# Optimization experiments

Measured on AMD Instinct MI355X. Metric: run time of the kernel, lower is better.

## Reference

```python
import jax, jax.numpy as jnp
import numpy as np

K_H, K_W = 3, 3
STRIDE, PAD = 1, 1
GN_GROUPS = 32
EPS = 1e-5


def setup_inputs() -> dict:
    key = jax.random.key(0)
    k1, k2, k3 = jax.random.split(key, 3)
    B, C, H, W = 4, 256, 64, 64
    Cout = 256
    x = jax.random.normal(k1, (B, C, H, W), jnp.float32)
    offset = jax.random.normal(k2, (B, 2 * K_H * K_W, H, W), jnp.float32)
    weight = jax.random.normal(k3, (Cout, C, K_H, K_W), jnp.float32) * 0.02
    gamma = jnp.ones((Cout,), jnp.float32)
    beta = jnp.zeros((Cout,), jnp.float32)
    return {"x": x, "offset": offset, "weight": weight, "gamma": gamma, "beta": beta}


def _deform_conv(x, offset, weight):
    B, C, H, W = x.shape
    Cout = weight.shape[0]
    K = K_H * K_W
    Ho = (H + 2 * PAD - K_H) // STRIDE + 1
    Wo = (W + 2 * PAD - K_W) // STRIDE + 1
    ky, kx = jnp.meshgrid(jnp.arange(K_H), jnp.arange(K_W), indexing='ij')
    ky = ky.reshape(K).astype(x.dtype)
    kx = kx.reshape(K).astype(x.dtype)
    # base sampling positions per kernel tap
    py_base = (jnp.arange(Ho) * STRIDE - PAD).astype(x.dtype)[None, :] + ky[:, None]  # [K,Ho]
    px_base = (jnp.arange(Wo) * STRIDE - PAD).astype(x.dtype)[None, :] + kx[:, None]  # [K,Wo]
    off = offset.reshape(B, K, 2, Ho, Wo)  # mmcv layout: (dy, dx) pairs per tap
    py = py_base[None, :, :, None] + off[:, :, 0]  # [B,K,Ho,Wo]
    px = px_base[None, :, None, :] + off[:, :, 1]  # [B,K,Ho,Wo]
    y0 = jnp.floor(py)
    x0 = jnp.floor(px)
    ly = py - y0
    lx = px - x0
    xf = x.reshape(B, C, H * W)

    def gather(yi, xi):
        valid = (yi >= 0) & (yi <= H - 1) & (xi >= 0) & (xi <= W - 1)
        yc = jnp.clip(yi, 0, H - 1).astype(jnp.int32)
        xc = jnp.clip(xi, 0, W - 1).astype(jnp.int32)
        idx = yc * W + xc  # [B,K,Ho,Wo]
        vals = jax.vmap(lambda xb, ib: xb[:, ib])(xf, idx)  # [B,C,K,Ho,Wo]
        return vals * valid[:, None].astype(x.dtype)

    g00 = gather(y0, x0)
    g01 = gather(y0, x0 + 1)
    g10 = gather(y0 + 1, x0)
    g11 = gather(y0 + 1, x0 + 1)
    wy = ly[:, None]  # [B,1,K,Ho,Wo]
    wx = lx[:, None]
    val = ((1 - wy) * (1 - wx) * g00 + (1 - wy) * wx * g01
           + wy * (1 - wx) * g10 + wy * wx * g11)  # [B,C,K,Ho,Wo]
    return jnp.einsum('bckhw,ock->bohw', val, weight.reshape(Cout, C, K))


def reference(x, offset, weight, gamma, beta):
    y = _deform_conv(x, offset, weight)  # [B,Cout,Ho,Wo]
    B, C, H, W = y.shape
    yg = y.reshape(B, GN_GROUPS, C // GN_GROUPS, H, W)
    mean = jnp.mean(yg, axis=(2, 3, 4), keepdims=True)
    var = jnp.var(yg, axis=(2, 3, 4), keepdims=True)
    yn = ((yg - mean) * jax.lax.rsqrt(var + EPS)).reshape(B, C, H, W)
    out = yn * gamma[None, :, None, None] + beta[None, :, None, None]
    return jax.nn.relu(out)
```

## Files before the change

### kernel.cpp

```cpp
#include <hip/hip_runtime.h>

typedef unsigned short ushort_t;
typedef __bf16 bf16x8 __attribute__((ext_vector_type(8)));
typedef float f32x4 __attribute__((ext_vector_type(4)));
typedef void __attribute__((address_space(1))) gvoid_t;
typedef void __attribute__((address_space(3))) lvoid_t;

__device__ __forceinline__ float bflo(unsigned u) { return __builtin_bit_cast(float, u << 16); }
__device__ __forceinline__ float bfhi(unsigned u) { return __builtin_bit_cast(float, u & 0xffff0000u); }
__device__ __forceinline__ float bf2f(ushort_t v) {
  return __builtin_bit_cast(float, ((unsigned)v) << 16);
}
__device__ __forceinline__ unsigned f2bf_bits(float f) {
  unsigned u = __builtin_bit_cast(unsigned, f);
  return (u + 0x7fffu + ((u >> 16) & 1u)) >> 16;
}
__device__ __forceinline__ ushort_t f2bf(float f) { return (ushort_t)f2bf_bits(f); }

__global__ __launch_bounds__(256) void k_prep(const float* __restrict__ x,
                                              const float* __restrict__ w,
                                              ushort_t* __restrict__ xt,
                                              ushort_t* __restrict__ wb,
                                              float* __restrict__ stats) {
  const int gid = blockIdx.x;
  const int t = threadIdx.x;
  if (gid >= 1024) {
    if (gid == 1024) stats[t] = 0.f;
    const int idx = (gid - 1024) * 256 + t;
    const float* src = w + (size_t)idx * 9;
    #pragma unroll
    for (int k = 0; k < 9; ++k)
      wb[(k << 16) + idx] = f2bf(src[k]);
    return;
  }
  __shared__ ushort_t tile[64][68];
  const int b = gid >> 8;
  const int ct = (gid >> 6) & 3;
  const int pt = gid & 63;
  const float* xb = x + ((size_t)(b * 256 + ct * 64)) * 4096 + pt * 64;
  #pragma unroll
  for (int i = 0; i < 16; ++i) {
    const int idx = t + 256 * i;
    const int c_l = idx >> 6, p_l = idx & 63;
    tile[c_l][p_l] = f2bf(xb[(size_t)c_l * 4096 + p_l]);
  }
  __syncthreads();
  ushort_t* xo = xt + ((size_t)(b * 4096 + pt * 64)) * 256 + ct * 64;
  #pragma unroll
  for (int i = 0; i < 16; ++i) {
    const int idx = t + 256 * i;
    const int p_l = idx >> 6, c_l = idx & 63;
    xo[(size_t)p_l * 256 + c_l] = tile[c_l][p_l];
  }
}

struct SMeta {
  float w00, w01, w10, w11;
  int i00, i01, i10, i11;
};
__device__ __forceinline__ SMeta meta_for(int h, int gw, int k, float oy, float ox) {
  SMeta m;
  const float py = (float)(h - 1 + k / 3) + oy;
  const float px = (float)(gw - 1 + k % 3) + ox;
  const float fy = floorf(py), fx = floorf(px);
  const float ly = py - fy, lx = px - fx;
  const int iy0 = (int)fy, ix0 = (int)fx;
  const float vy0 = (iy0 >= 0 && iy0 < 64) ? 1.f : 0.f;
  const float vy1 = (iy0 >= -1 && iy0 < 63) ? 1.f : 0.f;
  const float vx0 = (ix0 >= 0 && ix0 < 64) ? 1.f : 0.f;
  const float vx1 = (ix0 >= -1 && ix0 < 63) ? 1.f : 0.f;
  m.w00 = (1.f - ly) * (1.f - lx) * vy0 * vx0;
  m.w01 = (1.f - ly) * lx * vy0 * vx1;
  m.w10 = ly * (1.f - lx) * vy1 * vx0;
  m.w11 = ly * lx * vy1 * vx1;
  const int cy0 = min(max(iy0, 0), 63), cy1 = min(max(iy0 + 1, 0), 63);
  const int cx0 = min(max(ix0, 0), 63), cx1 = min(max(ix0 + 1, 0), 63);
  m.i00 = (cy0 * 64 + cx0) * 256;
  m.i01 = (cy0 * 64 + cx1) * 256;
  m.i10 = (cy1 * 64 + cx0) * 256;
  m.i11 = (cy1 * 64 + cx1) * 256;
  return m;
}

__device__ __forceinline__ unsigned lerp_pack(unsigned a, unsigned b, unsigned c, unsigned d,
                                              float w00, float w01, float w10, float w11) {
  float lo = w00 * bflo(a) + w01 * bflo(b) + w10 * bflo(c) + w11 * bflo(d);
  float hi = w00 * bfhi(a) + w01 * bfhi(b) + w10 * bfhi(c) + w11 * bfhi(d);
  return f2bf_bits(lo) | (f2bf_bits(hi) << 16);
}

template <int KH>
__device__ __forceinline__ void run_gemm(const float* __restrict__ offb,
                                         const ushort_t* __restrict__ xtb,
                                         const ushort_t* __restrict__ wb,
                                         ushort_t* Ab, ushort_t* Bb,
                                         int h, int s_w, int c8, int t,
                                         int wm, int wn, int wq, int wr,
                                         f32x4 (&acc)[2][4]) {
  float oy[5], ox[5];
  #pragma unroll
  for (int i = 0; i < 5; ++i) {
    oy[i] = offb[(2 * (KH * 4 + i)) * 4096];
    ox[i] = offb[(2 * (KH * 4 + i) + 1) * 4096];
  }

#define GATHER(N)                                                \
  {                                                              \
    const int c_ = KH * 18 + (N);                                \
    const int tap_ = c_ >> 2;                                    \
    const int loc_ = tap_ - KH * 4;                              \
    const int c0_ = (c_ & 3) << 6;                               \
    m = meta_for(h, s_w, tap_, oy[loc_], ox[loc_]);              \
    const int cc_ = c0_ + c8 * 8;                                \
    q00 = *(const uint4*)(xtb + m.i00 + cc_);                    \
    q01 = *(const uint4*)(xtb + m.i01 + cc_);                    \
    q10 = *(const uint4*)(xtb + m.i10 + cc_);                    \
    q11 = *(const uint4*)(xtb + m.i11 + cc_);                    \
  }

#define B_ISSUE(N, BUF)                                                                        \
  {                                                                                            \
    const int c_ = KH * 18 + (N);                                                              \
    const int tap_ = c_ >> 2;                                                                  \
    const int c0_ = (c_ & 3) << 6;                                                             \
    _Pragma("unroll") for (int i_ = 0; i_ < 4; ++i_) {                                         \
      const int idx_ = i_ * 512 + t;                                                           \
      const int row_ = idx_ >> 3, slot_ = idx_ & 7;                                            \
      const ushort_t* g_ = wb + (tap_ << 16) + row_ * 256 + c0_ + ((slot_ ^ (row_ & 7)) << 3); \
      __builtin_amdgcn_global_load_lds(                                                        \
          (gvoid_t*)g_, (lvoid_t*)((char*)Bb + (BUF) * 32768 + idx_ * 16), 16, 0, 0);          \
    }                                                                                          \
  }

#define A_WRITE(BUF)                                                         \
  {                                                                          \
    uint4 r;                                                                 \
    r.x = lerp_pack(q00.x, q01.x, q10.x, q11.x, m.w00, m.w01, m.w10, m.w11); \
    r.y = lerp_pack(q00.y, q01.y, q10.y, q11.y, m.w00, m.w01, m.w10, m.w11); \
    r.z = lerp_pack(q00.z, q01.z, q10.z, q11.z, m.w00, m.w01, m.w10, m.w11); \
    r.w = lerp_pack(q00.w, q01.w, q10.w, q11.w, m.w00, m.w01, m.w10, m.w11); \
    *(uint4*)&Ab[(BUF) * 4096 + s_w * 64 + ((c8 ^ (s_w & 7)) << 3)] = r;     \
  }

  {
    SMeta m;
    uint4 q00, q01, q10, q11;
    B_ISSUE(0, 0);
    GATHER(0);
    A_WRITE(0);
  }
  __syncthreads();

  #pragma unroll
  for (int n = 0; n < 18; ++n) {
    const int cur = n & 1;
    const int nb = cur ^ 1;
    SMeta m;
    uint4 q00, q01, q10, q11;
    if (n < 17) {
      B_ISSUE(n + 1, nb);
      GATHER(n + 1);
    }
    #pragma unroll
    for (int ks = 0; ks < 2; ++ks) {
      bf16x8 af[2], bfr[4];
      #pragma unroll
      for (int tm = 0; tm < 2; ++tm) {
        const int row = wm * 32 + tm * 16 + wr;
        const int slot = (ks * 4 + wq) ^ (row & 7);
        af[tm] = *(const bf16x8*)&Ab[cur * 4096 + row * 64 + slot * 8];
      }
      #pragma unroll
      for (int tn = 0; tn < 4; ++tn) {
        const int row = wn * 64 + tn * 16 + wr;
        const int slot = (ks * 4 + wq) ^ (row & 7);
        bfr[tn] = *(const bf16x8*)&Bb[cur * 16384 + row * 64 + slot * 8];
      }
      __builtin_amdgcn_s_setprio(1);
      #pragma unroll
      for (int tm = 0; tm < 2; ++tm)
        #pragma unroll
        for (int tn = 0; tn < 4; ++tn)
          acc[tm][tn] =
              __builtin_amdgcn_mfma_f32_16x16x32_bf16(af[tm], bfr[tn], acc[tm][tn], 0, 0, 0);
      __builtin_amdgcn_s_setprio(0);
    }
    if (n < 17) {
      A_WRITE(nb);
      __syncthreads();
    }
  }
#undef GATHER
#undef B_ISSUE
#undef A_WRITE
}

__global__ __launch_bounds__(512) void k_gemm(const float* __restrict__ off,
                                              const ushort_t* __restrict__ xt,
                                              const ushort_t* __restrict__ wb,
                                              ushort_t* __restrict__ y0,
                                              ushort_t* __restrict__ y1) {
  __shared__ __attribute__((aligned(16))) ushort_t Abuf[2][64 * 64];
  __shared__ __attribute__((aligned(16))) ushort_t Bbuf[2][256 * 64];

  const int bid = blockIdx.x;
  const int rowid = bid & 255;
  const int kh = bid >> 8;
  const int lb = ((rowid & 7) << 5) | (rowid >> 3);
  const int b = lb >> 6;
  const int h = lb & 63;
  const int t = threadIdx.x;
  const int wave = t >> 6;
  const int lane = t & 63;
  const int wq = lane >> 4;
  const int wr = lane & 15;
  const int wm = wave >> 2;
  const int wn = wave & 3;
  const int s_w = t >> 3;
  const int c8 = t & 7;

  const f32x4 zero = {0.f, 0.f, 0.f, 0.f};
  f32x4 acc[2][4];
  #pragma unroll
  for (int i = 0; i < 2; ++i)
    #pragma unroll
    for (int j = 0; j < 4; ++j) acc[i][j] = zero;

  const ushort_t* xtb = xt + (size_t)b * 4096 * 256;
  const float* offb = off + (size_t)b * 18 * 4096 + h * 64 + s_w;

  if (kh == 0)
    run_gemm<0>(offb, xtb, wb, &Abuf[0][0], &Bbuf[0][0], h, s_w, c8, t, wm, wn, wq, wr, acc);
  else
    run_gemm<1>(offb, xtb, wb, &Abuf[0][0], &Bbuf[0][0], h, s_w, c8, t, wm, wn, wq, wr, acc);

  ushort_t* yb = (kh ? y1 : y0) + ((size_t)(b * 4096 + h * 64)) * 256;
  #pragma unroll
  for (int tm = 0; tm < 2; ++tm) {
    #pragma unroll
    for (int tn = 0; tn < 4; ++tn) {
      const int o = wn * 64 + tn * 16 + wr;
      #pragma unroll
      for (int r2 = 0; r2 < 4; ++r2) {
        const int ww = wm * 32 + tm * 16 + wq * 4 + r2;
        yb[ww * 256 + o] = f2bf(acc[tm][tn][r2]);
      }
    }
  }
}

__global__ __launch_bounds__(256) void k_comb(const ushort_t* __restrict__ y0,
                                              const ushort_t* __restrict__ y1,
                                              ushort_t* __restrict__ yc,
                                              float* __restrict__ stats) {
  __shared__ float tile[64][65];
  const int bid = blockIdx.x;
  const int lb = ((bid & 7) << 7) | (bid >> 3);
  const int b = lb >> 8;
  const int st = (lb >> 2) & 63;
  const int ot = lb & 3;
  const int t = threadIdx.x;
  const size_t ybase = ((size_t)(b * 4096 + st * 64)) * 256 + ot * 64;
  float sum = 0.f, ss = 0.f;
  #pragma unroll
  for (int i = 0; i < 2; ++i) {
    const int u = t + 256 * i;
    const int s_l = u >> 3;
    const int o8 = u & 7;
    const size_t adr = ybase + (size_t)s_l * 256 + o8 * 8;
    const uint4 a = *(const uint4*)(y0 + adr);
    const uint4 c = *(const uint4*)(y1 + adr);
    float v[8];
    v[0] = bflo(a.x) + bflo(c.x); v[1] = bfhi(a.x) + bfhi(c.x);
    v[2] = bflo(a.y) + bflo(c.y); v[3] = bfhi(a.y) + bfhi(c.y);
    v[4] = bflo(a.z) + bflo(c.z); v[5] = bfhi(a.z) + bfhi(c.z);
    v[6] = bflo(a.w) + bflo(c.w); v[7] = bfhi(a.w) + bfhi(c.w);
    #pragma unroll
    for (int j = 0; j < 8; ++j) {
      sum += v[j];
      ss += v[j] * v[j];
      tile[s_l][o8 * 8 + j] = v[j];
    }
  }
  #pragma unroll
  for (int d = 8; d < 64; d <<= 1) {
    sum += __shfl_xor(sum, d, 64);
    ss += __shfl_xor(ss, d, 64);
  }
  if ((t & 63) < 8) {
    const int g = ot * 8 + (t & 7);
    atomicAdd(&stats[(b * 32 + g) * 2], sum);
    atomicAdd(&stats[(b * 32 + g) * 2 + 1], ss);
  }
  __syncthreads();
  #pragma unroll
  for (int i = 0; i < 2; ++i) {
    const int u = t + 256 * i;
    const int o_l = u >> 3;
    const int s8 = u & 7;
    float v[8];
    #pragma unroll
    for (int j = 0; j < 8; ++j) v[j] = tile[s8 * 8 + j][o_l];
    uint4 r;
    r.x = f2bf_bits(v[0]) | (f2bf_bits(v[1]) << 16);
    r.y = f2bf_bits(v[2]) | (f2bf_bits(v[3]) << 16);
    r.z = f2bf_bits(v[4]) | (f2bf_bits(v[5]) << 16);
    r.w = f2bf_bits(v[6]) | (f2bf_bits(v[7]) << 16);
    *(uint4*)(yc + ((size_t)(b * 256 + ot * 64 + o_l)) * 4096 + st * 64 + s8 * 8) = r;
  }
}

__global__ __launch_bounds__(256) void k_apply(const ushort_t* __restrict__ yc,
                                               const float* __restrict__ stats,
                                               const float* __restrict__ gamma,
                                               const float* __restrict__ beta,
                                               float* __restrict__ out) {
  const int bid = blockIdx.x;
  const int lb = ((bid & 7) << 8) | (bid >> 3);
  const size_t base = (size_t)lb * 2048 + threadIdx.x * 8;
  const int b = (int)(base >> 20);
  const int o = (int)((base >> 12) & 255);
  const int g = o >> 3;
  const float s1 = stats[(b * 32 + g) * 2];
  const float s2 = stats[(b * 32 + g) * 2 + 1];
  const float mean = s1 * (1.f / 32768.f);
  const float var = s2 * (1.f / 32768.f) - mean * mean;
  const float rstd = rsqrtf(var + 1e-5f);
  const float sc = rstd * gamma[o];
  const float sh = beta[o] - mean * sc;
  const uint4 a = *(const uint4*)(yc + base);
  float v[8];
  v[0] = bflo(a.x); v[1] = bfhi(a.x);
  v[2] = bflo(a.y); v[3] = bfhi(a.y);
  v[4] = bflo(a.z); v[5] = bfhi(a.z);
  v[6] = bflo(a.w); v[7] = bfhi(a.w);
  float4 f0, f1;
  f0.x = fmaxf(v[0] * sc + sh, 0.f);
  f0.y = fmaxf(v[1] * sc + sh, 0.f);
  f0.z = fmaxf(v[2] * sc + sh, 0.f);
  f0.w = fmaxf(v[3] * sc + sh, 0.f);
  f1.x = fmaxf(v[4] * sc + sh, 0.f);
  f1.y = fmaxf(v[5] * sc + sh, 0.f);
  f1.z = fmaxf(v[6] * sc + sh, 0.f);
  f1.w = fmaxf(v[7] * sc + sh, 0.f);
  *(float4*)(out + base) = f0;
  *(float4*)(out + base + 4) = f1;
}

extern "C" void kernel_launch(void* const* d_in, const int* in_sizes, int n_in,
                              void* d_out, int out_size, void* d_ws, size_t ws_size,
                              hipStream_t stream) {
  const float* x = (const float*)d_in[0];
  const float* off = (const float*)d_in[1];
  const float* w = (const float*)d_in[2];
  const float* gamma = (const float*)d_in[3];
  const float* beta = (const float*)d_in[4];
  float* out = (float*)d_out;

  char* ws = (char*)d_ws;
  ushort_t* y0 = (ushort_t*)(ws);
  ushort_t* y1 = (ushort_t*)(ws + 8388608);
  ushort_t* xt = (ushort_t*)(ws + 16777216);
  ushort_t* yc = xt;
  ushort_t* wb = (ushort_t*)(ws + 25165824);
  float* stats = (float*)(ws + 26345472);

  k_prep<<<1280, 256, 0, stream>>>(x, w, xt, wb, stats);
  k_gemm<<<512, 512, 0, stream>>>(off, xt, wb, y0, y1);
  k_comb<<<1024, 256, 0, stream>>>(y0, y1, yc, stats);
  k_apply<<<2048, 256, 0, stream>>>(yc, stats, gamma, beta, out);
}
```

Baseline: 85.51 us.

## Fuse split-K combine and GN stats into GEMM via last-block flag, merge apply with transpose

The separate combine kernel is removed. The second of the two split-K GEMM blocks for each row, detected with an atomic counter per row, sums y0 and y1, writes the combined bf16 result back into y0, and accumulates the group-norm statistics. The apply kernel now reads the channel-last y0 directly, normalises it, applies ReLU and transposes through shared memory into the NCHW output. This removes one launch and one round trip of the intermediate tensor through memory, at the cost of threadfences and extra tail work in the GEMM. The MFMA setprio hints are also dropped.

```diff
diff --git a/kernel.cpp b/kernel.cpp
--- a/kernel.cpp
+++ b/kernel.cpp
@@ -8,9 +8,6 @@
 
 __device__ __forceinline__ float bflo(unsigned u) { return __builtin_bit_cast(float, u << 16); }
 __device__ __forceinline__ float bfhi(unsigned u) { return __builtin_bit_cast(float, u & 0xffff0000u); }
-__device__ __forceinline__ float bf2f(ushort_t v) {
-  return __builtin_bit_cast(float, ((unsigned)v) << 16);
-}
 __device__ __forceinline__ unsigned f2bf_bits(float f) {
   unsigned u = __builtin_bit_cast(unsigned, f);
   return (u + 0x7fffu + ((u >> 16) & 1u)) >> 16;
@@ -21,11 +18,13 @@
                                               const float* __restrict__ w,
                                               ushort_t* __restrict__ xt,
                                               ushort_t* __restrict__ wb,
-                                              float* __restrict__ stats) {
+                                              float* __restrict__ stats,
+                                              int* __restrict__ flags) {
   const int gid = blockIdx.x;
   const int t = threadIdx.x;
   if (gid >= 1024) {
     if (gid == 1024) stats[t] = 0.f;
+    if (gid == 1025) flags[t] = 0;
     const int idx = (gid - 1024) * 256 + t;
     const float* src = w + (size_t)idx * 9;
     #pragma unroll
@@ -176,14 +175,12 @@
         const int slot = (ks * 4 + wq) ^ (row & 7);
         bfr[tn] = *(const bf16x8*)&Bb[cur * 16384 + row * 64 + slot * 8];
       }
-      __builtin_amdgcn_s_setprio(1);
       #pragma unroll
       for (int tm = 0; tm < 2; ++tm)
         #pragma unroll
         for (int tn = 0; tn < 4; ++tn)
           acc[tm][tn] =
               __builtin_amdgcn_mfma_f32_16x16x32_bf16(af[tm], bfr[tn], acc[tm][tn], 0, 0, 0);
-      __builtin_amdgcn_s_setprio(0);
     }
     if (n < 17) {
       A_WRITE(nb);
@@ -199,7 +196,9 @@
                                               const ushort_t* __restrict__ xt,
                                               const ushort_t* __restrict__ wb,
                                               ushort_t* __restrict__ y0,
-                                              ushort_t* __restrict__ y1) {
+                                              ushort_t* __restrict__ y1,
+                                              float* __restrict__ stats,
+                                              int* __restrict__ flags) {
   __shared__ __attribute__((aligned(16))) ushort_t Abuf[2][64 * 64];
   __shared__ __attribute__((aligned(16))) ushort_t Bbuf[2][256 * 64];
 
@@ -234,7 +233,8 @@
   else
     run_gemm<1>(offb, xtb, wb, &Abuf[0][0], &Bbuf[0][0], h, s_w, c8, t, wm, wn, wq, wr, acc);
 
-  ushort_t* yb = (kh ? y1 : y0) + ((size_t)(b * 4096 + h * 64)) * 256;
+  const size_t rowb = ((size_t)(b * 4096 + h * 64)) * 256;
+  ushort_t* yb = (kh ? y1 : y0) + rowb;
   #pragma unroll
   for (int tm = 0; tm < 2; ++tm) {
     #pragma unroll
@@ -247,12 +247,57 @@
       }
     }
   }
-}
-
-__global__ __launch_bounds__(256) void k_comb(const ushort_t* __restrict__ y0,
-                                              const ushort_t* __restrict__ y1,
-                                              ushort_t* __restrict__ yc,
-                                              float* __restrict__ stats) {
+
+  __threadfence();
+  int* fsh = (int*)&Abuf[0][0];
+  if (t == 0) *fsh = atomicAdd(&flags[rowid], 1);
+  __syncthreads();
+  const int second = *fsh;
+  if (second == 1) {
+    __threadfence();
+    const int s_l = t >> 3;
+    const int o8 = t & 7;
+    #pragma unroll
+    for (int ot = 0; ot < 4; ++ot) {
+      const size_t adr = rowb + (size_t)s_l * 256 + ot * 64 + o8 * 8;
+      const uint4 a = *(const uint4*)(y0 + adr);
+      const uint4 c = *(const uint4*)(y1 + adr);
+      float v[8];
+      v[0] = bflo(a.x) + bflo(c.x); v[1] = bfhi(a.x) + bfhi(c.x);
+      v[2] = bflo(a.y) + bflo(c.y); v[3] = bfhi(a.y) + bfhi(c.y);
+      v[4] = bflo(a.z) + bflo(c.z); v[5] = bfhi(a.z) + bfhi(c.z);
+      v[6] = bflo(a.w) + bflo(c.w); v[7] = bfhi(a.w) + bfhi(c.w);
+      float sum = 0.f, ss = 0.f;
+      #pragma unroll
+      for (int j = 0; j < 8; ++j) {
+        sum += v[j];
+        ss += v[j] * v[j];
+      }
+      uint4 r;
+      r.x = f2bf_bits(v[0]) | (f2bf_bits(v[1]) << 16);
+      r.y = f2bf_bits(v[2]) | (f2bf_bits(v[3]) << 16);
+      r.z = f2bf_bits(v[4]) | (f2bf_bits(v[5]) << 16);
+      r.w = f2bf_bits(v[6]) | (f2bf_bits(v[7]) << 16);
+      *(uint4*)(y0 + adr) = r;
+      #pragma unroll
+      for (int d = 8; d < 64; d <<= 1) {
+        sum += __shfl_xor(sum, d, 64);
+        ss += __shfl_xor(ss, d, 64);
+      }
+      if (lane < 8) {
+        const int g = ot * 8 + lane;
+        atomicAdd(&stats[(b * 32 + g) * 2], sum);
+        atomicAdd(&stats[(b * 32 + g) * 2 + 1], ss);
+      }
+    }
+  }
+}
+
+__global__ __launch_bounds__(256) void k_apply(const ushort_t* __restrict__ yc,
+                                               const float* __restrict__ stats,
+                                               const float* __restrict__ gamma,
+                                               const float* __restrict__ beta,
+                                               float* __restrict__ out) {
   __shared__ float tile[64][65];
   const int bid = blockIdx.x;
   const int lb = ((bid & 7) << 7) | (bid >> 3);
@@ -260,37 +305,31 @@
   const int st = (lb >> 2) & 63;
   const int ot = lb & 3;
   const int t = threadIdx.x;
-  const size_t ybase = ((size_t)(b * 4096 + st * 64)) * 256 + ot * 64;
-  float sum = 0.f, ss = 0.f;
   #pragma unroll
   for (int i = 0; i < 2; ++i) {
     const int u = t + 256 * i;
     const int s_l = u >> 3;
     const int o8 = u & 7;
-    const size_t adr = ybase + (size_t)s_l * 256 + o8 * 8;
-    const uint4 a = *(const uint4*)(y0 + adr);
-    const uint4 c = *(const uint4*)(y1 + adr);
+    const size_t adr = ((size_t)(b * 4096 + st * 64 + s_l)) * 256 + ot * 64 + o8 * 8;
+    const uint4 a = *(const uint4*)(yc + adr);
     float v[8];
-    v[0] = bflo(a.x) + bflo(c.x); v[1] = bfhi(a.x) + bfhi(c.x);
-    v[2] = bflo(a.y) + bflo(c.y); v[3] = bfhi(a.y) + bfhi(c.y);
-    v[4] = bflo(a.z) + bflo(c.z); v[5] = bfhi(a.z) + bfhi(c.z);
-    v[6] = bflo(a.w) + bflo(c.w); v[7] = bfhi(a.w) + bfhi(c.w);
+    v[0] = bflo(a.x); v[1] = bfhi(a.x);
+    v[2] = bflo(a.y); v[3] = bfhi(a.y);
+    v[4] = bflo(a.z); v[5] = bfhi(a.z);
+    v[6] = bflo(a.w); v[7] = bfhi(a.w);
+    const int g = ot * 8 + o8;
+    const float s1 = stats[(b * 32 + g) * 2];
+    const float s2 = stats[(b * 32 + g) * 2 + 1];
+    const float mean = s1 * (1.f / 32768.f);
+    const float var = s2 * (1.f / 32768.f) - mean * mean;
+    const float rstd = rsqrtf(var + 1e-5f);
     #pragma unroll
     for (int j = 0; j < 8; ++j) {
-      sum += v[j];
-      ss += v[j] * v[j];
-      tile[s_l][o8 * 8 + j] = v[j];
-    }
-  }
-  #pragma unroll
-  for (int d = 8; d < 64; d <<= 1) {
-    sum += __shfl_xor(sum, d, 64);
-    ss += __shfl_xor(ss, d, 64);
-  }
-  if ((t & 63) < 8) {
-    const int g = ot * 8 + (t & 7);
-    atomicAdd(&stats[(b * 32 + g) * 2], sum);
-    atomicAdd(&stats[(b * 32 + g) * 2 + 1], ss);
+      const int o = ot * 64 + o8 * 8 + j;
+      const float sc = rstd * gamma[o];
+      const float sh = beta[o] - mean * sc;
+      tile[s_l][o8 * 8 + j] = fmaxf(v[j] * sc + sh, 0.f);
+    }
   }
   __syncthreads();
   #pragma unroll
@@ -298,53 +337,19 @@
     const int u = t + 256 * i;
     const int o_l = u >> 3;
     const int s8 = u & 7;
-    float v[8];
-    #pragma unroll
-    for (int j = 0; j < 8; ++j) v[j] = tile[s8 * 8 + j][o_l];
-    uint4 r;
-    r.x = f2bf_bits(v[0]) | (f2bf_bits(v[1]) << 16);
-    r.y = f2bf_bits(v[2]) | (f2bf_bits(v[3]) << 16);
-    r.z = f2bf_bits(v[4]) | (f2bf_bits(v[5]) << 16);
-    r.w = f2bf_bits(v[6]) | (f2bf_bits(v[7]) << 16);
-    *(uint4*)(yc + ((size_t)(b * 256 + ot * 64 + o_l)) * 4096 + st * 64 + s8 * 8) = r;
-  }
-}
-
-__global__ __launch_bounds__(256) void k_apply(const ushort_t* __restrict__ yc,
-                                               const float* __restrict__ stats,
-                                               const float* __restrict__ gamma,
-                                               const float* __restrict__ beta,
-                                               float* __restrict__ out) {
-  const int bid = blockIdx.x;
-  const int lb = ((bid & 7) << 8) | (bid >> 3);
-  const size_t base = (size_t)lb * 2048 + threadIdx.x * 8;
-  const int b = (int)(base >> 20);
-  const int o = (int)((base >> 12) & 255);
-  const int g = o >> 3;
-  const float s1 = stats[(b * 32 + g) * 2];
-  const float s2 = stats[(b * 32 + g) * 2 + 1];
-  const float mean = s1 * (1.f / 32768.f);
-  const float var = s2 * (1.f / 32768.f) - mean * mean;
-  const float rstd = rsqrtf(var + 1e-5f);
-  const float sc = rstd * gamma[o];
-  const float sh = beta[o] - mean * sc;
-  const uint4 a = *(const uint4*)(yc + base);
-  float v[8];
-  v[0] = bflo(a.x); v[1] = bfhi(a.x);
-  v[2] = bflo(a.y); v[3] = bfhi(a.y);
-  v[4] = bflo(a.z); v[5] = bfhi(a.z);
-  v[6] = bflo(a.w); v[7] = bfhi(a.w);
-  float4 f0, f1;
-  f0.x = fmaxf(v[0] * sc + sh, 0.f);
-  f0.y = fmaxf(v[1] * sc + sh, 0.f);
-  f0.z = fmaxf(v[2] * sc + sh, 0.f);
-  f0.w = fmaxf(v[3] * sc + sh, 0.f);
-  f1.x = fmaxf(v[4] * sc + sh, 0.f);
-  f1.y = fmaxf(v[5] * sc + sh, 0.f);
-  f1.z = fmaxf(v[6] * sc + sh, 0.f);
-  f1.w = fmaxf(v[7] * sc + sh, 0.f);
-  *(float4*)(out + base) = f0;
-  *(float4*)(out + base + 4) = f1;
+    float4 f0, f1;
+    f0.x = tile[s8 * 8 + 0][o_l];
+    f0.y = tile[s8 * 8 + 1][o_l];
+    f0.z = tile[s8 * 8 + 2][o_l];
+    f0.w = tile[s8 * 8 + 3][o_l];
+    f1.x = tile[s8 * 8 + 4][o_l];
+    f1.y = tile[s8 * 8 + 5][o_l];
+    f1.z = tile[s8 * 8 + 6][o_l];
+    f1.w = tile[s8 * 8 + 7][o_l];
+    float* ob = out + ((size_t)(b * 256 + ot * 64 + o_l)) * 4096 + st * 64 + s8 * 8;
+    *(float4*)ob = f0;
+    *(float4*)(ob + 4) = f1;
+  }
 }
 
 extern "C" void kernel_launch(void* const* d_in, const int* in_sizes, int n_in,
@@ -361,12 +366,11 @@
   ushort_t* y0 = (ushort_t*)(ws);
   ushort_t* y1 = (ushort_t*)(ws + 8388608);
   ushort_t* xt = (ushort_t*)(ws + 16777216);
-  ushort_t* yc = xt;
   ushort_t* wb = (ushort_t*)(ws + 25165824);
   float* stats = (float*)(ws + 26345472);
-
-  k_prep<<<1280, 256, 0, stream>>>(x, w, xt, wb, stats);
-  k_gemm<<<512, 512, 0, stream>>>(off, xt, wb, y0, y1);
-  k_comb<<<1024, 256, 0, stream>>>(y0, y1, yc, stats);
-  k_apply<<<2048, 256, 0, stream>>>(yc, stats, gamma, beta, out);
-}
+  int* flags = (int*)(ws + 26346496);
+
+  k_prep<<<1280, 256, 0, stream>>>(x, w, xt, wb, stats, flags);
+  k_gemm<<<512, 512, 0, stream>>>(off, xt, wb, y0, y1, stats, flags);
+  k_apply<<<1024, 256, 0, stream>>>(y0, stats, gamma, beta, out);
+}
```

After: 240.4 us. 2.81x slower.
